# Kernel optimization log

Hardware: AMD Instinct MI355X
Metric: run time of the kernel (lower is better)

Reference implementation:

```python
import jax, jax.numpy as jnp
import numpy as np

TEMPERATURE = 8.0  # sqrt(head_dim=64)


def sparsemax(z):
    """Sparsemax along the last axis (Martins & Astudillo 2016)."""
    S = z.shape[-1]
    z_sorted = -jnp.sort(-z, axis=-1)            # descending sort
    cs = jnp.cumsum(z_sorted, axis=-1)
    ks = jnp.arange(1, S + 1, dtype=z.dtype)
    support = 1.0 + ks * z_sorted > cs           # entries in the support set
    k_sup = jnp.sum(support, axis=-1, keepdims=True)  # support size >= 1
    tau = (jnp.take_along_axis(cs, k_sup - 1, axis=-1) - 1.0) / k_sup.astype(z.dtype)
    return jnp.maximum(z - tau, 0.0)


def setup_inputs() -> dict:
    key = jax.random.key(0)
    kq, kk, kv, km = jax.random.split(key, 4)
    B, Lq, Lk, D = 64, 1024, 1024, 64
    q = jax.random.normal(kq, (B, Lq, D), dtype=jnp.float32)
    k = jax.random.normal(kk, (B, Lk, D), dtype=jnp.float32)
    v = jax.random.normal(kv, (B, Lk, D), dtype=jnp.float32)
    mask = jax.random.randint(km, (B, Lq, Lk), 0, 2).astype(bool)  # True = masked out
    return {"q": q, "k": k, "v": v, "mask": mask}


def reference(q, k, v, mask):
    # scores: [B, Lq, Lk]
    attn = jnp.einsum('bqd,bkd->bqk', q / TEMPERATURE, k)
    # mask out disallowed keys with -inf
    attn = jnp.where(mask, -jnp.inf, attn)
    # rows where ALL keys are masked: set scores to 0 (avoids NaN in sparsemax)
    inf_mask = jnp.all(mask, axis=2, keepdims=True)  # [B, Lq, 1]
    attn = jnp.where(inf_mask, 0.0, attn)
    attn = sparsemax(attn)
    # zero out fully-masked rows again (dropout has p=0.0 -> identity in eval)
    attn = jnp.where(inf_mask, 0.0, attn)
    out = jnp.einsum('bqk,bkd->bqd', attn, v)
    return (out, attn)
```

## Files before the change

### kernel.cpp

```cpp
#include <hip/hip_runtime.h>
#include <float.h>


#define BATCH    64
#define SEQQ     1024
#define SEQK     1024
#define DHEAD    64

typedef short short8 __attribute__((ext_vector_type(8)));
typedef float f32x4  __attribute__((ext_vector_type(4)));

__device__ __forceinline__ unsigned short bf16_rne(float f) {
    unsigned u = __float_as_uint(f);
    u += 0x7fffu + ((u >> 16) & 1u);
    return (unsigned short)(u >> 16);
}

__device__ __forceinline__ void cvt_hilo8(const float* fv, float scale,
                                          short8* hi, short8* lo) {
    #pragma unroll
    for (int j = 0; j < 8; ++j) {
        float f = fv[j] * scale;
        unsigned short hb = bf16_rne(f);
        float hf = __uint_as_float((unsigned)hb << 16);
        (*hi)[j] = (short)hb;
        (*lo)[j] = (short)bf16_rne(f - hf);
    }
}

__global__ void detect_mask_fmt(const unsigned char* __restrict__ m,
                                int* __restrict__ flag) {
    __shared__ int s_found;
    if (threadIdx.x == 0) s_found = 0;
    __syncthreads();
    int found = 0;
    for (int o = threadIdx.x; o < 65536; o += 256) {
        if ((o & 3) != 0 && m[o] != 0) found = 1;
    }
    if (found) atomicOr(&s_found, 1);
    __syncthreads();
    if (threadIdx.x == 0) *flag = s_found;
}

__global__ __launch_bounds__(256) void score_kernel(
        const float* __restrict__ q, const float* __restrict__ k,
        float* __restrict__ attn) {
    const int lane = threadIdx.x & 63;
    const int wave = threadIdx.x >> 6;
    const int quad = lane >> 4;
    const int l15  = lane & 15;
    const int kt = blockIdx.x, qt = blockIdx.y, b = blockIdx.z;

    __shared__ unsigned short klds[2 * 128 * 64];

    const float* kbase = k + ((size_t)b * SEQK + kt * 128) * DHEAD;
    #pragma unroll
    for (int it = 0; it < 4; ++it) {
        int e   = threadIdx.x + 256 * it;
        int key = e >> 3, db = e & 7;
        const float4* src = (const float4*)(kbase + key * DHEAD + db * 8);
        float4 f0 = src[0], f1 = src[1];
        float fv[8] = {f0.x, f0.y, f0.z, f0.w, f1.x, f1.y, f1.z, f1.w};
        short8 hi, lo;
        cvt_hilo8(fv, 1.0f, &hi, &lo);
        int off = key * 64 + ((db ^ (key & 7)) * 8);
        *(short8*)(klds + off)        = hi;
        *(short8*)(klds + 8192 + off) = lo;
    }
    __syncthreads();

    const float* qrow =
        q + ((size_t)b * SEQQ + qt * 64 + wave * 16 + l15) * DHEAD;
    short8 a_hi[2], a_lo[2];
    #pragma unroll
    for (int kc = 0; kc < 2; ++kc) {
        const float4* src = (const float4*)(qrow + kc * 32 + quad * 8);
        float4 f0 = src[0], f1 = src[1];
        float fv[8] = {f0.x, f0.y, f0.z, f0.w, f1.x, f1.y, f1.z, f1.w};
        cvt_hilo8(fv, 0.125f, &a_hi[kc], &a_lo[kc]);
    }

    float* arow = attn + ((size_t)b * SEQQ + qt * 64 + wave * 16) * SEQK
                       + kt * 128;
    #pragma unroll
    for (int g = 0; g < 8; ++g) {
        int key = g * 16 + l15;
        short8 b_hi[2], b_lo[2];
        #pragma unroll
        for (int kc = 0; kc < 2; ++kc) {
            int db  = kc * 4 + quad;
            int off = key * 64 + ((db ^ (key & 7)) * 8);
            b_hi[kc] = *(const short8*)(klds + off);
            b_lo[kc] = *(const short8*)(klds + 8192 + off);
        }
        f32x4 acc = {0.f, 0.f, 0.f, 0.f};
        #pragma unroll
        for (int kc = 0; kc < 2; ++kc) {
            acc = __builtin_amdgcn_mfma_f32_16x16x32_bf16(a_hi[kc], b_hi[kc], acc, 0, 0, 0);
            acc = __builtin_amdgcn_mfma_f32_16x16x32_bf16(a_lo[kc], b_hi[kc], acc, 0, 0, 0);
            acc = __builtin_amdgcn_mfma_f32_16x16x32_bf16(a_hi[kc], b_lo[kc], acc, 0, 0, 0);
        }
        #pragma unroll
        for (int r = 0; r < 4; ++r)
            arow[(size_t)(quad * 4 + r) * SEQK + g * 16 + l15] = acc[r];
    }
}

__global__ __launch_bounds__(256) void sparsemax_pv(
        const float* __restrict__ v, const void* __restrict__ mask,
        const int* __restrict__ fmt_flag,
        float* __restrict__ out, float* __restrict__ attn) {
    const int lane = threadIdx.x & 63;
    const int wave = threadIdx.x >> 6;
    const int row  = blockIdx.x * 4 + wave;
    const int b    = row >> 10;
    float* arow = attn + (size_t)row * SEQK;
    const int mask_is_byte = fmt_flag ? *fmt_flag : 1;

    float s[16];
    #pragma unroll
    for (int t = 0; t < 4; ++t) {
        float4 f = ((const float4*)arow)[lane + 64 * t];
        s[4*t+0] = f.x; s[4*t+1] = f.y; s[4*t+2] = f.z; s[4*t+3] = f.w;
    }
    if (mask_is_byte) {
        const unsigned* m32 =
            (const unsigned*)((const unsigned char*)mask + (size_t)row * SEQK);
        #pragma unroll
        for (int t = 0; t < 4; ++t) {
            unsigned m = m32[lane + 64 * t];
            if (m & 0x000000ffu) s[4*t+0] = -FLT_MAX;
            if (m & 0x0000ff00u) s[4*t+1] = -FLT_MAX;
            if (m & 0x00ff0000u) s[4*t+2] = -FLT_MAX;
            if (m & 0xff000000u) s[4*t+3] = -FLT_MAX;
        }
    } else {
        const int4* m4 = (const int4*)((const int*)mask + (size_t)row * SEQK);
        #pragma unroll
        for (int t = 0; t < 4; ++t) {
            int4 m = m4[lane + 64 * t];
            if (m.x) s[4*t+0] = -FLT_MAX;
            if (m.y) s[4*t+1] = -FLT_MAX;
            if (m.z) s[4*t+2] = -FLT_MAX;
            if (m.w) s[4*t+3] = -FLT_MAX;
        }
    }

    float mx = -FLT_MAX;
    #pragma unroll
    for (int i = 0; i < 16; ++i) mx = fmaxf(mx, s[i]);
    #pragma unroll
    for (int off = 32; off >= 1; off >>= 1)
        mx = fmaxf(mx, __shfl_xor(mx, off, 64));

    if (mx <= -FLT_MAX) {
        float4 z = {0.f, 0.f, 0.f, 0.f};
        #pragma unroll
        for (int t = 0; t < 4; ++t) ((float4*)arow)[lane + 64 * t] = z;
        out[(size_t)row * DHEAD + lane] = 0.f;
        return;
    }

    float thr = mx - 1.0f, tau = 0.f;
    int cnt_prev = -1;
    for (int it = 0; it < 32; ++it) {
        float lsum = 0.f; int lcnt = 0;
        #pragma unroll
        for (int i = 0; i < 16; ++i)
            if (s[i] > thr) { lsum += s[i]; lcnt++; }
        #pragma unroll
        for (int off = 32; off >= 1; off >>= 1) {
            lsum += __shfl_xor(lsum, off, 64);
            lcnt += __shfl_xor(lcnt, off, 64);
        }
        tau = (lsum - 1.0f) / (float)lcnt;
        if (lcnt == cnt_prev) break;
        cnt_prev = lcnt;
        thr = tau;
    }

    float p[16];
    #pragma unroll
    for (int i = 0; i < 16; ++i) {
        float pv = s[i] - tau;
        p[i] = pv > 0.f ? pv : 0.f;
    }
    #pragma unroll
    for (int t = 0; t < 4; ++t) {
        float4 f = {p[4*t+0], p[4*t+1], p[4*t+2], p[4*t+3]};
        ((float4*)arow)[lane + 64 * t] = f;
    }

    const float* vbase = v + (size_t)b * SEQK * DHEAD;
    float oacc = 0.f;
    #pragma unroll
    for (int t = 0; t < 4; ++t) {
        #pragma unroll
        for (int c = 0; c < 4; ++c) {
            int i = 4 * t + c;
            unsigned long long mball = __ballot(p[i] > 0.f);
            while (mball) {
                int src = __ffsll(mball) - 1;
                mball &= mball - 1;
                float pj = __shfl(p[i], src);
                int key = 4 * (src + 64 * t) + c;
                oacc = fmaf(pj, vbase[(size_t)key * DHEAD + lane], oacc);
            }
        }
    }
    out[(size_t)row * DHEAD + lane] = oacc;
}

extern "C" void kernel_launch(void* const* d_in, const int* in_sizes, int n_in,
                              void* d_out, int out_size, void* d_ws, size_t ws_size,
                              hipStream_t stream) {
    const float* q = (const float*)d_in[0];
    const float* k = (const float*)d_in[1];
    const float* v = (const float*)d_in[2];
    const void*  m = d_in[3];

    float* out  = (float*)d_out;
    float* attn = out + (size_t)BATCH * SEQQ * DHEAD;

    int* flag = nullptr;
    if (ws_size >= sizeof(int)) {
        flag = (int*)d_ws;
        detect_mask_fmt<<<1, 256, 0, stream>>>((const unsigned char*)m, flag);
    }

    dim3 gridA(SEQK / 128, SEQQ / 64, BATCH);
    score_kernel<<<gridA, 256, 0, stream>>>(q, k, attn);

    sparsemax_pv<<<(BATCH * SEQQ) / 4, 256, 0, stream>>>(v, m, flag, out, attn);
}
```

Measured before the change: 719.7 us.

## Fuse score, sparsemax and PV into one kernel with candidate compaction

New measurement: 993.2 us. 38.0% more time.

```diff
diff --git a/kernel.cpp b/kernel.cpp
--- a/kernel.cpp
+++ b/kernel.cpp
@@ -2,10 +2,12 @@
 #include <float.h>
 
 
-#define BATCH    64
-#define SEQQ     1024
-#define SEQK     1024
-#define DHEAD    64
+#define BATCH  64
+#define SEQQ   1024
+#define SEQK   1024
+#define DHEAD  64
+#define CAP    96
+#define CSTR   97
 
 typedef short short8 __attribute__((ext_vector_type(8)));
 typedef float f32x4  __attribute__((ext_vector_type(4)));
@@ -42,35 +44,31 @@
     if (threadIdx.x == 0) *flag = s_found;
 }
 
-__global__ __launch_bounds__(256) void score_kernel(
+__global__ __launch_bounds__(256, 2) void fused_sparse_attn(
         const float* __restrict__ q, const float* __restrict__ k,
-        float* __restrict__ attn) {
+        const float* __restrict__ v, const void* __restrict__ mask,
+        const int* __restrict__ fmt_flag,
+        float* __restrict__ out, float* __restrict__ attn) {
     const int lane = threadIdx.x & 63;
     const int wave = threadIdx.x >> 6;
     const int quad = lane >> 4;
     const int l15  = lane & 15;
-    const int kt = blockIdx.x, qt = blockIdx.y, b = blockIdx.z;
+    const int qt = blockIdx.x, b = blockIdx.y;
+    const int rowbase = b * SEQQ + qt * 64 + wave * 16;
 
     __shared__ unsigned short klds[2 * 128 * 64];
-
-    const float* kbase = k + ((size_t)b * SEQK + kt * 128) * DHEAD;
-    #pragma unroll
-    for (int it = 0; it < 4; ++it) {
-        int e   = threadIdx.x + 256 * it;
-        int key = e >> 3, db = e & 7;
-        const float4* src = (const float4*)(kbase + key * DHEAD + db * 8);
-        float4 f0 = src[0], f1 = src[1];
-        float fv[8] = {f0.x, f0.y, f0.z, f0.w, f1.x, f1.y, f1.z, f1.w};
-        short8 hi, lo;
-        cvt_hilo8(fv, 1.0f, &hi, &lo);
-        int off = key * 64 + ((db ^ (key & 7)) * 8);
-        *(short8*)(klds + off)        = hi;
-        *(short8*)(klds + 8192 + off) = lo;
-    }
-    __syncthreads();
-
-    const float* qrow =
-        q + ((size_t)b * SEQQ + qt * 64 + wave * 16 + l15) * DHEAD;
+    __shared__ float          cval[64 * CSTR];
+    __shared__ unsigned short cidx[64 * CSTR];
+    __shared__ int            ccnt[64];
+    __shared__ float          smax[64];
+
+    if (threadIdx.x < 64) ccnt[threadIdx.x] = 0;
+
+    const int mask_is_byte = fmt_flag ? *fmt_flag : 1;
+    const unsigned char* m8  = (const unsigned char*)mask;
+    const int*           m32 = (const int*)mask;
+
+    const float* qrow = q + (size_t)(rowbase + l15) * DHEAD;
     short8 a_hi[2], a_lo[2];
     #pragma unroll
     for (int kc = 0; kc < 2; ++kc) {
@@ -80,135 +78,220 @@
         cvt_hilo8(fv, 0.125f, &a_hi[kc], &a_lo[kc]);
     }
 
-    float* arow = attn + ((size_t)b * SEQQ + qt * 64 + wave * 16) * SEQK
-                       + kt * 128;
-    #pragma unroll
-    for (int g = 0; g < 8; ++g) {
-        int key = g * 16 + l15;
-        short8 b_hi[2], b_lo[2];
-        #pragma unroll
-        for (int kc = 0; kc < 2; ++kc) {
-            int db  = kc * 4 + quad;
+    float rmax_reg[4] = {-FLT_MAX, -FLT_MAX, -FLT_MAX, -FLT_MAX};
+    const float* kb = k + (size_t)b * SEQK * DHEAD;
+
+    for (int kt = 0; kt < 8; ++kt) {
+        __syncthreads();
+        const float* kbase = kb + (size_t)kt * 128 * DHEAD;
+        #pragma unroll
+        for (int it = 0; it < 4; ++it) {
+            int e   = threadIdx.x + 256 * it;
+            int key = e >> 3, db = e & 7;
+            const float4* src = (const float4*)(kbase + key * DHEAD + db * 8);
+            float4 f0 = src[0], f1 = src[1];
+            float fv[8] = {f0.x, f0.y, f0.z, f0.w, f1.x, f1.y, f1.z, f1.w};
+            short8 hi, lo;
+            cvt_hilo8(fv, 1.0f, &hi, &lo);
             int off = key * 64 + ((db ^ (key & 7)) * 8);
-            b_hi[kc] = *(const short8*)(klds + off);
-            b_lo[kc] = *(const short8*)(klds + 8192 + off);
-        }
-        f32x4 acc = {0.f, 0.f, 0.f, 0.f};
-        #pragma unroll
-        for (int kc = 0; kc < 2; ++kc) {
-            acc = __builtin_amdgcn_mfma_f32_16x16x32_bf16(a_hi[kc], b_hi[kc], acc, 0, 0, 0);
-            acc = __builtin_amdgcn_mfma_f32_16x16x32_bf16(a_lo[kc], b_hi[kc], acc, 0, 0, 0);
-            acc = __builtin_amdgcn_mfma_f32_16x16x32_bf16(a_hi[kc], b_lo[kc], acc, 0, 0, 0);
-        }
+            *(short8*)(klds + off)        = hi;
+            *(short8*)(klds + 8192 + off) = lo;
+        }
+        __syncthreads();
+
+        float sacc[8][4];
+        #pragma unroll
+        for (int g = 0; g < 8; ++g) {
+            int key = g * 16 + l15;
+            short8 b_hi[2], b_lo[2];
+            #pragma unroll
+            for (int kc = 0; kc < 2; ++kc) {
+                int db  = kc * 4 + quad;
+                int off = key * 64 + ((db ^ (key & 7)) * 8);
+                b_hi[kc] = *(const short8*)(klds + off);
+                b_lo[kc] = *(const short8*)(klds + 8192 + off);
+            }
+            f32x4 acc = {0.f, 0.f, 0.f, 0.f};
+            #pragma unroll
+            for (int kc = 0; kc < 2; ++kc) {
+                acc = __builtin_amdgcn_mfma_f32_16x16x32_bf16(a_hi[kc], b_hi[kc], acc, 0, 0, 0);
+                acc = __builtin_amdgcn_mfma_f32_16x16x32_bf16(a_lo[kc], b_hi[kc], acc, 0, 0, 0);
+                acc = __builtin_amdgcn_mfma_f32_16x16x32_bf16(a_hi[kc], b_lo[kc], acc, 0, 0, 0);
+            }
+            int colg = kt * 128 + g * 16 + l15;
+            #pragma unroll
+            for (int r = 0; r < 4; ++r) {
+                int rowg = rowbase + quad * 4 + r;
+                bool mm = mask_is_byte
+                    ? (m8[(size_t)rowg * SEQK + colg] != 0)
+                    : (m32[(size_t)rowg * SEQK + colg] != 0);
+                sacc[g][r] = mm ? -FLT_MAX : acc[r];
+            }
+        }
+
+        #pragma unroll
+        for (int r = 0; r < 4; ++r) {
+            float tm = sacc[0][r];
+            #pragma unroll
+            for (int g = 1; g < 8; ++g) tm = fmaxf(tm, sacc[g][r]);
+            #pragma unroll
+            for (int off = 8; off >= 1; off >>= 1)
+                tm = fmaxf(tm, __shfl_xor(tm, off, 64));
+            rmax_reg[r] = fmaxf(rmax_reg[r], tm);
+        }
+
+        #pragma unroll
+        for (int g = 0; g < 8; ++g) {
+            #pragma unroll
+            for (int r = 0; r < 4; ++r) {
+                float sv = sacc[g][r];
+                if (sv > rmax_reg[r] - 1.0f) {
+                    int wrow = wave * 16 + quad * 4 + r;
+                    int pos = atomicAdd(&ccnt[wrow], 1);
+                    if (pos < CAP) {
+                        cval[wrow * CSTR + pos] = sv;
+                        cidx[wrow * CSTR + pos] =
+                            (unsigned short)(kt * 128 + g * 16 + l15);
+                    }
+                }
+            }
+        }
+
+        float4 z4 = {0.f, 0.f, 0.f, 0.f};
+        #pragma unroll
+        for (int rep = 0; rep < 8; ++rep) {
+            int linear = rep * 64 + lane;
+            int rl = linear >> 5, c4 = linear & 31;
+            *(float4*)(attn + (size_t)(rowbase + rl) * SEQK + kt * 128 + c4 * 4) = z4;
+        }
+    }
+
+    if (l15 == 0) {
         #pragma unroll
         for (int r = 0; r < 4; ++r)
-            arow[(size_t)(quad * 4 + r) * SEQK + g * 16 + l15] = acc[r];
-    }
-}
-
-__global__ __launch_bounds__(256) void sparsemax_pv(
-        const float* __restrict__ v, const void* __restrict__ mask,
-        const int* __restrict__ fmt_flag,
-        float* __restrict__ out, float* __restrict__ attn) {
-    const int lane = threadIdx.x & 63;
-    const int wave = threadIdx.x >> 6;
-    const int row  = blockIdx.x * 4 + wave;
-    const int b    = row >> 10;
-    float* arow = attn + (size_t)row * SEQK;
-    const int mask_is_byte = fmt_flag ? *fmt_flag : 1;
-
-    float s[16];
-    #pragma unroll
-    for (int t = 0; t < 4; ++t) {
-        float4 f = ((const float4*)arow)[lane + 64 * t];
-        s[4*t+0] = f.x; s[4*t+1] = f.y; s[4*t+2] = f.z; s[4*t+3] = f.w;
-    }
-    if (mask_is_byte) {
-        const unsigned* m32 =
-            (const unsigned*)((const unsigned char*)mask + (size_t)row * SEQK);
-        #pragma unroll
-        for (int t = 0; t < 4; ++t) {
-            unsigned m = m32[lane + 64 * t];
-            if (m & 0x000000ffu) s[4*t+0] = -FLT_MAX;
-            if (m & 0x0000ff00u) s[4*t+1] = -FLT_MAX;
-            if (m & 0x00ff0000u) s[4*t+2] = -FLT_MAX;
-            if (m & 0xff000000u) s[4*t+3] = -FLT_MAX;
-        }
-    } else {
-        const int4* m4 = (const int4*)((const int*)mask + (size_t)row * SEQK);
-        #pragma unroll
-        for (int t = 0; t < 4; ++t) {
-            int4 m = m4[lane + 64 * t];
-            if (m.x) s[4*t+0] = -FLT_MAX;
-            if (m.y) s[4*t+1] = -FLT_MAX;
-            if (m.z) s[4*t+2] = -FLT_MAX;
-            if (m.w) s[4*t+3] = -FLT_MAX;
-        }
-    }
-
-    float mx = -FLT_MAX;
-    #pragma unroll
-    for (int i = 0; i < 16; ++i) mx = fmaxf(mx, s[i]);
-    #pragma unroll
-    for (int off = 32; off >= 1; off >>= 1)
-        mx = fmaxf(mx, __shfl_xor(mx, off, 64));
-
-    if (mx <= -FLT_MAX) {
-        float4 z = {0.f, 0.f, 0.f, 0.f};
-        #pragma unroll
-        for (int t = 0; t < 4; ++t) ((float4*)arow)[lane + 64 * t] = z;
-        out[(size_t)row * DHEAD + lane] = 0.f;
-        return;
-    }
-
-    float thr = mx - 1.0f, tau = 0.f;
-    int cnt_prev = -1;
-    for (int it = 0; it < 32; ++it) {
-        float lsum = 0.f; int lcnt = 0;
-        #pragma unroll
-        for (int i = 0; i < 16; ++i)
-            if (s[i] > thr) { lsum += s[i]; lcnt++; }
-        #pragma unroll
-        for (int off = 32; off >= 1; off >>= 1) {
-            lsum += __shfl_xor(lsum, off, 64);
-            lcnt += __shfl_xor(lcnt, off, 64);
-        }
-        tau = (lsum - 1.0f) / (float)lcnt;
-        if (lcnt == cnt_prev) break;
-        cnt_prev = lcnt;
-        thr = tau;
-    }
-
-    float p[16];
-    #pragma unroll
-    for (int i = 0; i < 16; ++i) {
-        float pv = s[i] - tau;
-        p[i] = pv > 0.f ? pv : 0.f;
-    }
-    #pragma unroll
-    for (int t = 0; t < 4; ++t) {
-        float4 f = {p[4*t+0], p[4*t+1], p[4*t+2], p[4*t+3]};
-        ((float4*)arow)[lane + 64 * t] = f;
-    }
-
-    const float* vbase = v + (size_t)b * SEQK * DHEAD;
-    float oacc = 0.f;
-    #pragma unroll
-    for (int t = 0; t < 4; ++t) {
-        #pragma unroll
-        for (int c = 0; c < 4; ++c) {
-            int i = 4 * t + c;
-            unsigned long long mball = __ballot(p[i] > 0.f);
-            while (mball) {
-                int src = __ffsll(mball) - 1;
-                mball &= mball - 1;
-                float pj = __shfl(p[i], src);
-                int key = 4 * (src + 64 * t) + c;
-                oacc = fmaf(pj, vbase[(size_t)key * DHEAD + lane], oacc);
-            }
-        }
-    }
-    out[(size_t)row * DHEAD + lane] = oacc;
+            smax[wave * 16 + quad * 4 + r] = rmax_reg[r];
+    }
+    __syncthreads();
+
+    const float* vb = v + (size_t)b * SEQK * DHEAD;
+
+    for (int rl = 0; rl < 16; ++rl) {
+        const int wrow = wave * 16 + rl;
+        const int rowg = rowbase + rl;
+        const int n    = ccnt[wrow];
+        float* arow = attn + (size_t)rowg * SEQK;
+
+        if (n <= CAP) {
+            float tau;
+            if (n == 0) {
+                tau = FLT_MAX;
+            } else {
+                float mx = smax[wrow];
+                float c0 = (lane < n)      ? cval[wrow * CSTR + lane]      : -FLT_MAX;
+                float c1 = (lane + 64 < n) ? cval[wrow * CSTR + lane + 64] : -FLT_MAX;
+                float thr = mx - 1.0f;
+                int cnt_prev = -1;
+                tau = 0.f;
+                for (int it = 0; it < 32; ++it) {
+                    float lsum = 0.f; int lcnt = 0;
+                    if (c0 > thr) { lsum += c0; ++lcnt; }
+                    if (c1 > thr) { lsum += c1; ++lcnt; }
+                    #pragma unroll
+                    for (int off = 32; off >= 1; off >>= 1) {
+                        lsum += __shfl_xor(lsum, off, 64);
+                        lcnt += __shfl_xor(lcnt, off, 64);
+                    }
+                    tau = (lsum - 1.0f) / (float)lcnt;
+                    if (lcnt == cnt_prev) break;
+                    cnt_prev = lcnt;
+                    thr = tau;
+                }
+            }
+            float oacc = 0.f;
+            for (int e0 = 0; e0 < n; e0 += 8) {
+                float pv[8]; int ix[8];
+                #pragma unroll
+                for (int u = 0; u < 8; ++u) {
+                    int e = e0 + u;
+                    if (e < n) {
+                        pv[u] = cval[wrow * CSTR + e] - tau;
+                        ix[u] = cidx[wrow * CSTR + e];
+                    } else { pv[u] = 0.f; ix[u] = 0; }
+                }
+                float vv[8];
+                #pragma unroll
+                for (int u = 0; u < 8; ++u)
+                    vv[u] = vb[(size_t)ix[u] * DHEAD + lane];
+                #pragma unroll
+                for (int u = 0; u < 8; ++u) {
+                    float p = pv[u] > 0.f ? pv[u] : 0.f;
+                    oacc = fmaf(p, vv[u], oacc);
+                    if (pv[u] > 0.f && lane == 0) arow[ix[u]] = pv[u];
+                }
+            }
+            out[(size_t)rowg * DHEAD + lane] = oacc;
+        } else {
+            const float4* q4 = (const float4*)(q + (size_t)rowg * DHEAD);
+            float s[16];
+            float fmx = -FLT_MAX;
+            #pragma unroll 2
+            for (int t = 0; t < 16; ++t) {
+                const float4* k4 =
+                    (const float4*)(kb + (size_t)(lane + 64 * t) * DHEAD);
+                float a0 = 0.f, a1 = 0.f, a2 = 0.f, a3 = 0.f;
+                #pragma unroll
+                for (int i = 0; i < 16; ++i) {
+                    float4 kv = k4[i], qv = q4[i];
+                    a0 = fmaf(qv.x, kv.x, a0);
+                    a1 = fmaf(qv.y, kv.y, a1);
+                    a2 = fmaf(qv.z, kv.z, a2);
+                    a3 = fmaf(qv.w, kv.w, a3);
+                }
+                float acc = ((a0 + a1) + (a2 + a3)) * 0.125f;
+                bool mm = mask_is_byte
+                    ? (m8[(size_t)rowg * SEQK + lane + 64 * t] != 0)
+                    : (m32[(size_t)rowg * SEQK + lane + 64 * t] != 0);
+                s[t] = mm ? -FLT_MAX : acc;
+                fmx = fmaxf(fmx, s[t]);
+            }
+            #pragma unroll
+            for (int off = 32; off >= 1; off >>= 1)
+                fmx = fmaxf(fmx, __shfl_xor(fmx, off, 64));
+            float thr = fmx - 1.0f, tau = 0.f;
+            int cnt_prev = -1;
+            for (int it = 0; it < 32; ++it) {
+                float lsum = 0.f; int lcnt = 0;
+                #pragma unroll
+                for (int t = 0; t < 16; ++t)
+                    if (s[t] > thr) { lsum += s[t]; ++lcnt; }
+                #pragma unroll
+                for (int off = 32; off >= 1; off >>= 1) {
+                    lsum += __shfl_xor(lsum, off, 64);
+                    lcnt += __shfl_xor(lcnt, off, 64);
+                }
+                tau = (lsum - 1.0f) / (float)lcnt;
+                if (lcnt == cnt_prev) break;
+                cnt_prev = lcnt;
+                thr = tau;
+            }
+            float p[16];
+            float oacc = 0.f;
+            #pragma unroll
+            for (int t = 0; t < 16; ++t) {
+                float pvv = s[t] - tau;
+                p[t] = pvv > 0.f ? pvv : 0.f;
+                arow[lane + 64 * t] = p[t];
+                unsigned long long mball = __ballot(p[t] > 0.f);
+                while (mball) {
+                    int src = __ffsll(mball) - 1;
+                    mball &= mball - 1;
+                    float pj = __shfl(p[t], src);
+                    oacc = fmaf(pj, vb[(size_t)(src + 64 * t) * DHEAD + lane], oacc);
+                }
+            }
+            out[(size_t)rowg * DHEAD + lane] = oacc;
+        }
+    }
 }
 
 extern "C" void kernel_launch(void* const* d_in, const int* in_sizes, int n_in,
@@ -228,8 +311,6 @@
         detect_mask_fmt<<<1, 256, 0, stream>>>((const unsigned char*)m, flag);
     }
 
-    dim3 gridA(SEQK / 128, SEQQ / 64, BATCH);
-    score_kernel<<<gridA, 256, 0, stream>>>(q, k, attn);
-
-    sparsemax_pv<<<(BATCH * SEQQ) / 4, 256, 0, stream>>>(v, m, flag, out, attn);
-}
+    dim3 grid(SEQQ / 64, BATCH);
+    fused_sparse_attn<<<grid, 256, 0, stream>>>(q, k, v, m, flag, out, attn);
+}
```
